# Optimization experiments

Hardware: AMD Instinct MI355X
Metric: run time of the kernel (lower is better)

## Reference

```python
import jax, jax.numpy as jnp
import numpy as np

N = 524288
D = 256
NUM_SEGMENTS = 8192


def setup_inputs() -> dict:
    key = jax.random.key(0)
    k = jax.random.split(key, 6)
    s = 1.0 / np.sqrt(D)
    s2 = 1.0 / np.sqrt(2 * D)
    return {
        "x": jax.random.normal(k[0], (N, D), dtype=jnp.float32),
        "batch_index": jnp.sort(jax.random.randint(k[1], (N,), 0, NUM_SEGMENTS, dtype=jnp.int32)),
        "W1": jax.random.uniform(k[2], (D, D), jnp.float32, -s, s),
        "b1": jax.random.uniform(k[3], (D,), jnp.float32, -s, s),
        "Wp": jax.random.uniform(k[4], (D, 2 * D), jnp.float32, -s2, s2),
        "bp": jax.random.uniform(k[5], (D,), jnp.float32, -s2, s2),
    }


def reference(x, batch_index, W1, b1, Wp, bp):
    # prepool linear: [N, D]
    h = x @ W1.T + b1
    # scatter-mean over groups
    seg_sum = jax.ops.segment_sum(h, batch_index, num_segments=NUM_SEGMENTS)
    counts = jax.ops.segment_sum(jnp.ones((h.shape[0],), h.dtype), batch_index, num_segments=NUM_SEGMENTS)
    xmean = seg_sum / jnp.maximum(counts, 1.0)[:, None]
    # scatter-max over groups (empty segments -> 0, matching torch_scatter default fill; they are never gathered)
    xmax = jax.ops.segment_max(h, batch_index, num_segments=NUM_SEGMENTS)
    xmax = jnp.where(jnp.isfinite(xmax), xmax, jnp.zeros_like(xmax))
    # meanmax concat -> proj -> gather back to entities
    xpool = jnp.concatenate([xmean, xmax], axis=1)  # [B, 2D]
    out = xpool @ Wp.T + bp  # [B, D]
    return out[batch_index]  # [N, D]
```

## Files before the change

kernel.cpp:

```cpp
#include <hip/hip_runtime.h>
#include <hip/hip_bf16.h>

#define NROWS 524288
#define DIM 256
#define NSEG 8192
#define SPB 8
#define SEGS3 16

typedef __attribute__((ext_vector_type(8))) short bf16x8;
typedef __attribute__((ext_vector_type(4))) float f32x4;

__device__ __forceinline__ short f2bf(float f) {
  union { float f; unsigned u; } a; a.f = f;
  unsigned r = a.u + 0x7fffu + ((a.u >> 16) & 1u);
  return (short)(r >> 16);
}

__global__ void seg_start_kernel(const int* __restrict__ bi, int* __restrict__ ss) {
  int s = blockIdx.x * blockDim.x + threadIdx.x;
  if (s > NSEG) return;
  int lo = 0, hi = NROWS;
  while (lo < hi) { int mid = (lo + hi) >> 1; if (bi[mid] < s) lo = mid + 1; else hi = mid; }
  ss[s] = lo;
}

__global__ __launch_bounds__(256, 2) void gemm_pool_kernel(
    const float* __restrict__ x, const int* __restrict__ bi,
    const float* __restrict__ W1, const float* __restrict__ b1,
    const int* __restrict__ ss, float* __restrict__ xpool) {
  __shared__ short x_lds[16 * 264];
  __shared__ float hT[256 * 20];

  const int tid = threadIdx.x;
  const int wave = tid >> 6, lane = tid & 63;
  const int quad = lane >> 4, l16 = lane & 15;

  bf16x8 bfr[4][8];
  #pragma unroll
  for (int tt = 0; tt < 4; ++tt) {
    const int col = wave * 64 + tt * 16 + l16;
    #pragma unroll
    for (int ks = 0; ks < 8; ++ks) {
      const float* p = W1 + col * DIM + ks * 32 + quad * 8;
      f32x4 w0 = *(const f32x4*)p;
      f32x4 w1 = *(const f32x4*)(p + 4);
      bf16x8 f;
      f[0]=f2bf(w0[0]); f[1]=f2bf(w0[1]); f[2]=f2bf(w0[2]); f[3]=f2bf(w0[3]);
      f[4]=f2bf(w1[0]); f[5]=f2bf(w1[1]); f[6]=f2bf(w1[2]); f[7]=f2bf(w1[3]);
      bfr[tt][ks] = f;
    }
  }
  const float b1v = b1[tid];
  const int r0 = ss[blockIdx.x * SPB];
  const int r1 = ss[blockIdx.x * SPB + SPB];
  if (r0 >= r1) return;

  int cur = bi[r0];
  float run_sum = 0.f, run_max = -3.0e38f;
  const int srow = tid >> 4;
  const int scol = (tid & 15) * 16;

  for (int base = r0; base < r1; base += 16) {
    int nr = r1 - base; if (nr > 16) nr = 16;
    if (srow < nr) {
      const float* xp = x + (size_t)(base + srow) * DIM + scol;
      f32x4 v0 = *(const f32x4*)xp;
      f32x4 v1 = *(const f32x4*)(xp + 4);
      f32x4 v2 = *(const f32x4*)(xp + 8);
      f32x4 v3 = *(const f32x4*)(xp + 12);
      bf16x8 s0, s1;
      s0[0]=f2bf(v0[0]); s0[1]=f2bf(v0[1]); s0[2]=f2bf(v0[2]); s0[3]=f2bf(v0[3]);
      s0[4]=f2bf(v1[0]); s0[5]=f2bf(v1[1]); s0[6]=f2bf(v1[2]); s0[7]=f2bf(v1[3]);
      s1[0]=f2bf(v2[0]); s1[1]=f2bf(v2[1]); s1[2]=f2bf(v2[2]); s1[3]=f2bf(v2[3]);
      s1[4]=f2bf(v3[0]); s1[5]=f2bf(v3[1]); s1[6]=f2bf(v3[2]); s1[7]=f2bf(v3[3]);
      *(bf16x8*)&x_lds[srow * 264 + scol] = s0;
      *(bf16x8*)&x_lds[srow * 264 + scol + 8] = s1;
    }
    __syncthreads();
    bf16x8 af[8];
    #pragma unroll
    for (int ks = 0; ks < 8; ++ks)
      af[ks] = *(const bf16x8*)&x_lds[l16 * 264 + ks * 32 + quad * 8];
    f32x4 acc[4];
    #pragma unroll
    for (int tt = 0; tt < 4; ++tt) {
      f32x4 a = {0.f, 0.f, 0.f, 0.f};
      #pragma unroll
      for (int ks = 0; ks < 8; ++ks)
        a = __builtin_amdgcn_mfma_f32_16x16x32_bf16(af[ks], bfr[tt][ks], a, 0, 0, 0);
      acc[tt] = a;
    }
    #pragma unroll
    for (int tt = 0; tt < 4; ++tt) {
      const int col = wave * 64 + tt * 16 + l16;
      *(f32x4*)&hT[col * 20 + quad * 4] = acc[tt];
    }
    __syncthreads();
    f32x4 h0 = *(const f32x4*)&hT[tid * 20 + 0];
    f32x4 h1 = *(const f32x4*)&hT[tid * 20 + 4];
    f32x4 h2 = *(const f32x4*)&hT[tid * 20 + 8];
    f32x4 h3 = *(const f32x4*)&hT[tid * 20 + 12];
    float hv[16] = {h0[0],h0[1],h0[2],h0[3], h1[0],h1[1],h1[2],h1[3],
                    h2[0],h2[1],h2[2],h2[3], h3[0],h3[1],h3[2],h3[3]};
    #pragma unroll
    for (int r = 0; r < 16; ++r) {
      if (r < nr) {
        int s = bi[base + r];
        if (s != cur) {
          int cnt = ss[cur + 1] - ss[cur];
          xpool[(size_t)cur * 512 + tid]       = run_sum / (float)cnt + b1v;
          xpool[(size_t)cur * 512 + 256 + tid] = run_max + b1v;
          cur = s; run_sum = 0.f; run_max = -3.0e38f;
        }
        run_sum += hv[r];
        run_max = fmaxf(run_max, hv[r]);
      }
    }
  }
  {
    int cnt = ss[cur + 1] - ss[cur];
    xpool[(size_t)cur * 512 + tid]       = run_sum / (float)cnt + b1v;
    xpool[(size_t)cur * 512 + 256 + tid] = run_max + b1v;
  }
}

__global__ __launch_bounds__(256) void proj_kernel(
    const float* __restrict__ xpool, const float* __restrict__ Wp,
    const float* __restrict__ bp, float* __restrict__ out_pool) {
  __shared__ float xp_lds[SEGS3 * 512];
  const int tid = threadIdx.x;
  const size_t s0 = (size_t)blockIdx.x * SEGS3;
  for (int i = tid; i < SEGS3 * 128; i += 256)
    *(f32x4*)&xp_lds[i * 4] = *(const f32x4*)&xpool[s0 * 512 + (size_t)i * 4];
  __syncthreads();
  float acc[SEGS3];
  #pragma unroll
  for (int s = 0; s < SEGS3; ++s) acc[s] = 0.f;
  for (int k0 = 0; k0 < 512; k0 += 4) {
    f32x4 wp = *(const f32x4*)&Wp[(size_t)tid * 512 + k0];
    #pragma unroll
    for (int s = 0; s < SEGS3; ++s) {
      f32x4 xv = *(const f32x4*)&xp_lds[s * 512 + k0];
      acc[s] += xv[0]*wp[0] + xv[1]*wp[1] + xv[2]*wp[2] + xv[3]*wp[3];
    }
  }
  const float b = bp[tid];
  #pragma unroll
  for (int s = 0; s < SEGS3; ++s)
    out_pool[(s0 + s) * 256 + tid] = acc[s] + b;
}

__global__ void gather_kernel(const int* __restrict__ bi,
                              const float* __restrict__ out_pool,
                              float* __restrict__ out) {
  const size_t idx = (size_t)blockIdx.x * blockDim.x + threadIdx.x;
  const int n  = (int)(idx >> 6);
  const int c4 = (int)(idx & 63);
  const int s = bi[n];
  f32x4 v = *(const f32x4*)&out_pool[(size_t)s * 256 + c4 * 4];
  *(f32x4*)&out[(size_t)n * 256 + (size_t)c4 * 4] = v;
}

extern "C" void kernel_launch(void* const* d_in, const int* in_sizes, int n_in,
                              void* d_out, int out_size, void* d_ws, size_t ws_size,
                              hipStream_t stream) {
  const float* x  = (const float*)d_in[0];
  const int*   bi = (const int*)d_in[1];
  const float* W1 = (const float*)d_in[2];
  const float* b1 = (const float*)d_in[3];
  const float* Wp = (const float*)d_in[4];
  const float* bp = (const float*)d_in[5];
  float* out = (float*)d_out;

  char* ws = (char*)d_ws;
  int*   ss       = (int*)ws;
  float* xpool    = (float*)(ws + 64 * 1024);
  float* out_pool = (float*)(ws + 64 * 1024 + (size_t)NSEG * 512 * 4);

  seg_start_kernel<<<(NSEG + 256) / 256, 256, 0, stream>>>(bi, ss);
  gemm_pool_kernel<<<NSEG / SPB, 256, 0, stream>>>(x, bi, W1, b1, ss, xpool);
  proj_kernel<<<NSEG / SEGS3, 256, 0, stream>>>(xpool, Wp, bp, out_pool);
  gather_kernel<<<(size_t)NROWS * (DIM / 4) / 256, 256, 0, stream>>>(bi, out_pool, out);
}
```

Before: 1.101 ms.

## Double-buffer x tiles and reduce segments directly from MFMA accumulators

The gemm_pool kernel now prefetches the next 16-row tile of x into registers while the MFMAs for the current tile run, using two LDS buffers and one barrier per chunk. The per-row serial scan through the hT transpose in LDS is replaced by segment-range logic driven by the segment starts: sums and maxes are reduced straight from the MFMA accumulators, with a fast path for chunks lying wholly inside one segment and cross-quad shuffles at segment boundaries. It also removes per-row batch_index reads and halves the proj kernel's segments per block to launch more blocks. The cost is more complex control flow with a data-dependent inner while loop and higher register pressure.

```diff
diff --git a/kernel.cpp b/kernel.cpp
--- a/kernel.cpp
+++ b/kernel.cpp
@@ -1,11 +1,10 @@
 #include <hip/hip_runtime.h>
-#include <hip/hip_bf16.h>
 
 #define NROWS 524288
 #define DIM 256
 #define NSEG 8192
 #define SPB 8
-#define SEGS3 16
+#define SEGS3 8
 
 typedef __attribute__((ext_vector_type(8))) short bf16x8;
 typedef __attribute__((ext_vector_type(4))) float f32x4;
@@ -25,15 +24,19 @@
 }
 
 __global__ __launch_bounds__(256, 2) void gemm_pool_kernel(
-    const float* __restrict__ x, const int* __restrict__ bi,
-    const float* __restrict__ W1, const float* __restrict__ b1,
-    const int* __restrict__ ss, float* __restrict__ xpool) {
-  __shared__ short x_lds[16 * 264];
-  __shared__ float hT[256 * 20];
-
-  const int tid = threadIdx.x;
+    const float* __restrict__ x, const float* __restrict__ W1,
+    const float* __restrict__ b1, const int* __restrict__ ss,
+    float* __restrict__ xpool) {
+  __shared__ short x_lds[2][16 * 264];
+
+  const int tid  = threadIdx.x;
   const int wave = tid >> 6, lane = tid & 63;
   const int quad = lane >> 4, l16 = lane & 15;
+
+  const int s0i = blockIdx.x * SPB;
+  const int r0 = ss[s0i];
+  const int r1 = ss[s0i + SPB];
+  if (r0 >= r1) return;
 
   bf16x8 bfr[4][8];
   #pragma unroll
@@ -41,7 +44,7 @@
     const int col = wave * 64 + tt * 16 + l16;
     #pragma unroll
     for (int ks = 0; ks < 8; ++ks) {
-      const float* p = W1 + col * DIM + ks * 32 + quad * 8;
+      const float* p = W1 + (size_t)col * DIM + ks * 32 + quad * 8;
       f32x4 w0 = *(const f32x4*)p;
       f32x4 w1 = *(const f32x4*)(p + 4);
       bf16x8 f;
@@ -50,77 +53,124 @@
       bfr[tt][ks] = f;
     }
   }
-  const float b1v = b1[tid];
-  const int r0 = ss[blockIdx.x * SPB];
-  const int r1 = ss[blockIdx.x * SPB + SPB];
-  if (r0 >= r1) return;
-
-  int cur = bi[r0];
-  float run_sum = 0.f, run_max = -3.0e38f;
+  const float b1f = b1[wave * 64 + quad * 16 + l16];
+
   const int srow = tid >> 4;
   const int scol = (tid & 15) * 16;
 
-  for (int base = r0; base < r1; base += 16) {
-    int nr = r1 - base; if (nr > 16) nr = 16;
-    if (srow < nr) {
-      const float* xp = x + (size_t)(base + srow) * DIM + scol;
+  {
+    const int row = r0 + srow;
+    if (row < r1) {
+      const float* xp = x + (size_t)row * DIM + scol;
       f32x4 v0 = *(const f32x4*)xp;
       f32x4 v1 = *(const f32x4*)(xp + 4);
       f32x4 v2 = *(const f32x4*)(xp + 8);
       f32x4 v3 = *(const f32x4*)(xp + 12);
-      bf16x8 s0, s1;
-      s0[0]=f2bf(v0[0]); s0[1]=f2bf(v0[1]); s0[2]=f2bf(v0[2]); s0[3]=f2bf(v0[3]);
-      s0[4]=f2bf(v1[0]); s0[5]=f2bf(v1[1]); s0[6]=f2bf(v1[2]); s0[7]=f2bf(v1[3]);
-      s1[0]=f2bf(v2[0]); s1[1]=f2bf(v2[1]); s1[2]=f2bf(v2[2]); s1[3]=f2bf(v2[3]);
-      s1[4]=f2bf(v3[0]); s1[5]=f2bf(v3[1]); s1[6]=f2bf(v3[2]); s1[7]=f2bf(v3[3]);
-      *(bf16x8*)&x_lds[srow * 264 + scol] = s0;
-      *(bf16x8*)&x_lds[srow * 264 + scol + 8] = s1;
+      bf16x8 a0, a1;
+      a0[0]=f2bf(v0[0]); a0[1]=f2bf(v0[1]); a0[2]=f2bf(v0[2]); a0[3]=f2bf(v0[3]);
+      a0[4]=f2bf(v1[0]); a0[5]=f2bf(v1[1]); a0[6]=f2bf(v1[2]); a0[7]=f2bf(v1[3]);
+      a1[0]=f2bf(v2[0]); a1[1]=f2bf(v2[1]); a1[2]=f2bf(v2[2]); a1[3]=f2bf(v2[3]);
+      a1[4]=f2bf(v3[0]); a1[5]=f2bf(v3[1]); a1[6]=f2bf(v3[2]); a1[7]=f2bf(v3[3]);
+      *(bf16x8*)&x_lds[0][srow * 264 + scol] = a0;
+      *(bf16x8*)&x_lds[0][srow * 264 + scol + 8] = a1;
+    }
+  }
+  __syncthreads();
+
+  int idx = 0;
+  int seg_lo = r0;
+  int seg_hi = ss[s0i + 1];
+  while (seg_hi == seg_lo) { ++idx; seg_lo = seg_hi; seg_hi = ss[s0i + idx + 1]; }
+
+  float ssum[4] = {0.f, 0.f, 0.f, 0.f};
+  float smax[4] = {-3.0e38f, -3.0e38f, -3.0e38f, -3.0e38f};
+
+  const int nch = (r1 - r0 + 15) >> 4;
+  for (int c = 0; c < nch; ++c) {
+    const int base = r0 + c * 16;
+    int nr = r1 - base; if (nr > 16) nr = 16;
+
+    f32x4 v0, v1, v2, v3;
+    const int prow = base + 16 + srow;
+    const bool pf = (prow < r1);
+    if (pf) {
+      const float* xp = x + (size_t)prow * DIM + scol;
+      v0 = *(const f32x4*)xp;
+      v1 = *(const f32x4*)(xp + 4);
+      v2 = *(const f32x4*)(xp + 8);
+      v3 = *(const f32x4*)(xp + 12);
+    }
+
+    const short* xb = x_lds[c & 1];
+    f32x4 acc[4] = {{0.f,0.f,0.f,0.f},{0.f,0.f,0.f,0.f},{0.f,0.f,0.f,0.f},{0.f,0.f,0.f,0.f}};
+    #pragma unroll
+    for (int ks = 0; ks < 8; ++ks) {
+      bf16x8 a = *(const bf16x8*)&xb[l16 * 264 + ks * 32 + quad * 8];
+      acc[0] = __builtin_amdgcn_mfma_f32_16x16x32_bf16(a, bfr[0][ks], acc[0], 0, 0, 0);
+      acc[1] = __builtin_amdgcn_mfma_f32_16x16x32_bf16(a, bfr[1][ks], acc[1], 0, 0, 0);
+      acc[2] = __builtin_amdgcn_mfma_f32_16x16x32_bf16(a, bfr[2][ks], acc[2], 0, 0, 0);
+      acc[3] = __builtin_amdgcn_mfma_f32_16x16x32_bf16(a, bfr[3][ks], acc[3], 0, 0, 0);
+    }
+
+    int r = 0;
+    while (r < nr) {
+      int e = seg_hi - base; if (e > nr) e = nr;
+      if (r == 0 && e == 16) {
+        #pragma unroll
+        for (int tt = 0; tt < 4; ++tt) {
+          ssum[tt] += (acc[tt][0] + acc[tt][1]) + (acc[tt][2] + acc[tt][3]);
+          smax[tt] = fmaxf(smax[tt], fmaxf(fmaxf(acc[tt][0], acc[tt][1]),
+                                           fmaxf(acc[tt][2], acc[tt][3])));
+        }
+      } else {
+        #pragma unroll
+        for (int tt = 0; tt < 4; ++tt) {
+          #pragma unroll
+          for (int j = 0; j < 4; ++j) {
+            const int row = (quad << 2) + j;
+            const bool in = (row >= r) && (row < e);
+            ssum[tt] += in ? acc[tt][j] : 0.f;
+            smax[tt] = in ? fmaxf(smax[tt], acc[tt][j]) : smax[tt];
+          }
+        }
+      }
+      if (base + e == seg_hi) {
+        float c0 = ssum[0], c1 = ssum[1], c2 = ssum[2], c3 = ssum[3];
+        c0 += __shfl_xor(c0, 16); c0 += __shfl_xor(c0, 32);
+        c1 += __shfl_xor(c1, 16); c1 += __shfl_xor(c1, 32);
+        c2 += __shfl_xor(c2, 16); c2 += __shfl_xor(c2, 32);
+        c3 += __shfl_xor(c3, 16); c3 += __shfl_xor(c3, 32);
+        float m0 = smax[0], m1 = smax[1], m2 = smax[2], m3 = smax[3];
+        m0 = fmaxf(m0, __shfl_xor(m0, 16)); m0 = fmaxf(m0, __shfl_xor(m0, 32));
+        m1 = fmaxf(m1, __shfl_xor(m1, 16)); m1 = fmaxf(m1, __shfl_xor(m1, 32));
+        m2 = fmaxf(m2, __shfl_xor(m2, 16)); m2 = fmaxf(m2, __shfl_xor(m2, 32));
+        m3 = fmaxf(m3, __shfl_xor(m3, 16)); m3 = fmaxf(m3, __shfl_xor(m3, 32));
+        const float fs = (quad & 2) ? ((quad & 1) ? c3 : c2) : ((quad & 1) ? c1 : c0);
+        const float fm = (quad & 2) ? ((quad & 1) ? m3 : m2) : ((quad & 1) ? m1 : m0);
+        const float inv = 1.f / (float)(seg_hi - seg_lo);
+        const int col = wave * 64 + quad * 16 + l16;
+        xpool[(size_t)(s0i + idx) * 512 + col]       = fs * inv + b1f;
+        xpool[(size_t)(s0i + idx) * 512 + 256 + col] = fm + b1f;
+        ssum[0]=0.f; ssum[1]=0.f; ssum[2]=0.f; ssum[3]=0.f;
+        smax[0]=-3.0e38f; smax[1]=-3.0e38f; smax[2]=-3.0e38f; smax[3]=-3.0e38f;
+        if (base + e < r1) {
+          do { ++idx; seg_lo = seg_hi; seg_hi = ss[s0i + idx + 1]; } while (seg_hi == seg_lo);
+        }
+      }
+      r = e;
+    }
+
+    if (pf) {
+      bf16x8 a0, a1;
+      a0[0]=f2bf(v0[0]); a0[1]=f2bf(v0[1]); a0[2]=f2bf(v0[2]); a0[3]=f2bf(v0[3]);
+      a0[4]=f2bf(v1[0]); a0[5]=f2bf(v1[1]); a0[6]=f2bf(v1[2]); a0[7]=f2bf(v1[3]);
+      a1[0]=f2bf(v2[0]); a1[1]=f2bf(v2[1]); a1[2]=f2bf(v2[2]); a1[3]=f2bf(v2[3]);
+      a1[4]=f2bf(v3[0]); a1[5]=f2bf(v3[1]); a1[6]=f2bf(v3[2]); a1[7]=f2bf(v3[3]);
+      short* dst = &x_lds[(c + 1) & 1][srow * 264 + scol];
+      *(bf16x8*)dst = a0;
+      *(bf16x8*)(dst + 8) = a1;
     }
     __syncthreads();
-    bf16x8 af[8];
-    #pragma unroll
-    for (int ks = 0; ks < 8; ++ks)
-      af[ks] = *(const bf16x8*)&x_lds[l16 * 264 + ks * 32 + quad * 8];
-    f32x4 acc[4];
-    #pragma unroll
-    for (int tt = 0; tt < 4; ++tt) {
-      f32x4 a = {0.f, 0.f, 0.f, 0.f};
-      #pragma unroll
-      for (int ks = 0; ks < 8; ++ks)
-        a = __builtin_amdgcn_mfma_f32_16x16x32_bf16(af[ks], bfr[tt][ks], a, 0, 0, 0);
-      acc[tt] = a;
-    }
-    #pragma unroll
-    for (int tt = 0; tt < 4; ++tt) {
-      const int col = wave * 64 + tt * 16 + l16;
-      *(f32x4*)&hT[col * 20 + quad * 4] = acc[tt];
-    }
-    __syncthreads();
-    f32x4 h0 = *(const f32x4*)&hT[tid * 20 + 0];
-    f32x4 h1 = *(const f32x4*)&hT[tid * 20 + 4];
-    f32x4 h2 = *(const f32x4*)&hT[tid * 20 + 8];
-    f32x4 h3 = *(const f32x4*)&hT[tid * 20 + 12];
-    float hv[16] = {h0[0],h0[1],h0[2],h0[3], h1[0],h1[1],h1[2],h1[3],
-                    h2[0],h2[1],h2[2],h2[3], h3[0],h3[1],h3[2],h3[3]};
-    #pragma unroll
-    for (int r = 0; r < 16; ++r) {
-      if (r < nr) {
-        int s = bi[base + r];
-        if (s != cur) {
-          int cnt = ss[cur + 1] - ss[cur];
-          xpool[(size_t)cur * 512 + tid]       = run_sum / (float)cnt + b1v;
-          xpool[(size_t)cur * 512 + 256 + tid] = run_max + b1v;
-          cur = s; run_sum = 0.f; run_max = -3.0e38f;
-        }
-        run_sum += hv[r];
-        run_max = fmaxf(run_max, hv[r]);
-      }
-    }
-  }
-  {
-    int cnt = ss[cur + 1] - ss[cur];
-    xpool[(size_t)cur * 512 + tid]       = run_sum / (float)cnt + b1v;
-    xpool[(size_t)cur * 512 + 256 + tid] = run_max + b1v;
   }
 }
 
@@ -150,7 +200,7 @@
     out_pool[(s0 + s) * 256 + tid] = acc[s] + b;
 }
 
-__global__ void gather_kernel(const int* __restrict__ bi,
+__global__ __launch_bounds__(256) void gather_kernel(const int* __restrict__ bi,
                               const float* __restrict__ out_pool,
                               float* __restrict__ out) {
   const size_t idx = (size_t)blockIdx.x * blockDim.x + threadIdx.x;
@@ -178,7 +228,7 @@
   float* out_pool = (float*)(ws + 64 * 1024 + (size_t)NSEG * 512 * 4);
 
   seg_start_kernel<<<(NSEG + 256) / 256, 256, 0, stream>>>(bi, ss);
-  gemm_pool_kernel<<<NSEG / SPB, 256, 0, stream>>>(x, bi, W1, b1, ss, xpool);
+  gemm_pool_kernel<<<NSEG / SPB, 256, 0, stream>>>(x, W1, b1, ss, xpool);
   proj_kernel<<<NSEG / SEGS3, 256, 0, stream>>>(xpool, Wp, bp, out_pool);
   gather_kernel<<<(size_t)NROWS * (DIM / 4) / 256, 256, 0, stream>>>(bi, out_pool, out);
 }
```

Result: faster. 1.074 ms (-2.5%).
